# Optimization experiments

Hardware: AMD Instinct MI355X
Metric: run time of the kernel (lower is better)

Reference implementation:

```python
import jax, jax.numpy as jnp
import numpy as np

VOCAB, E, H, L, B, T, S, V = 32000, 512, 1024, 2, 64, 64, 128, 1024
LSTM_IN = 2 * E  # input_feed=True -> cat(embed, prev_output)


def setup_inputs() -> dict:
    key = jax.random.key(0)
    ks = jax.random.split(key, 12)
    s = lambda *d: 1.0 / np.sqrt(d[-1])
    return {
        "tgt_batch": jax.random.randint(ks[0], (T, B), 0, VOCAB),
        "h_encoder": jax.random.normal(ks[1], (B, S, V), jnp.float32),
        "emb": jax.random.normal(ks[2], (VOCAB, E), jnp.float32) * 0.02,
        "output_init": jnp.zeros((B, E), jnp.float32),
        "hidden_init": jnp.zeros((L, B, H), jnp.float32),
        "W_ih": jax.random.uniform(ks[3], (L, 4 * H, LSTM_IN), jnp.float32, -s(H), s(H)),
        "W_hh": jax.random.uniform(ks[4], (L, 4 * H, H), jnp.float32, -s(H), s(H)),
        "b_ih": jax.random.uniform(ks[5], (L, 4 * H), jnp.float32, -s(H), s(H)),
        "b_hh": jax.random.uniform(ks[6], (L, 4 * H), jnp.float32, -s(H), s(H)),
        "W1": jax.random.uniform(ks[7], (V, H), jnp.float32, -s(H), s(H)),   # query_size->values_size
        "b1": jnp.zeros((V,), jnp.float32),
        "W2": jax.random.uniform(ks[8], (E, H + V), jnp.float32, -s(H + V), s(H + V)),
        "b2": jnp.zeros((E,), jnp.float32),
    }


def reference(tgt_batch, h_encoder, emb, output_init, hidden_init,
              W_ih, W_hh, b_ih, b_hh, W1, b1, W2, b2):
    x_seq = emb[tgt_batch]  # [T, B, E]

    def lstm_cell(x, h, c):  # x:[B,2E], h/c:[L,B,H]
        hs, cs, inp = [], [], x
        for l in range(L):
            gates = inp @ W_ih[l].T + b_ih[l] + h[l] @ W_hh[l].T + b_hh[l]
            i, f, g, o = jnp.split(gates, 4, axis=-1)  # torch gate order i,f,g,o
            c_new = jax.nn.sigmoid(f) * c[l] + jax.nn.sigmoid(i) * jnp.tanh(g)
            h_new = jax.nn.sigmoid(o) * jnp.tanh(c_new)
            hs.append(h_new); cs.append(c_new); inp = h_new
        return jnp.stack(hs), jnp.stack(cs), inp

    def global_attn(query):  # query:[B,H]
        q = query @ W1.T + b1                              # [B,V]
        scores = jnp.einsum('bv,bsv->bs', q, h_encoder)    # [B,S]
        a = jax.nn.softmax(scores, axis=-1)
        attended = jnp.einsum('bs,bsv->bv', a, h_encoder)  # [B,V]
        return jnp.tanh(jnp.concatenate([attended, query], axis=-1) @ W2.T + b2)

    def step(carry, x):
        h, c, out = carry
        inp = jnp.concatenate([x, out], axis=-1)  # input feed
        h, c, top = lstm_cell(inp, h, c)
        o = global_attn(top)  # dropout is identity in eval mode
        return (h, c, o), o

    c0 = jnp.zeros_like(hidden_init)
    _, outs = jax.lax.scan(step, (hidden_init, c0, output_init), x_seq)
    return jnp.transpose(outs, (1, 0, 2))  # [B, T, E]
```

## Files before the change

kernel.cpp:

```cpp
#include <hip/hip_runtime.h>

typedef _Float16 f16;
typedef f16 f16x8 __attribute__((ext_vector_type(8)));
typedef f16 f16x2 __attribute__((ext_vector_type(2)));
typedef float f32x4 __attribute__((ext_vector_type(4)));
typedef unsigned long long u64;

#define MFMA16(a, b, c) __builtin_amdgcn_mfma_f32_16x16x32_f16(a, b, c, 0, 0, 0)
#define ROT 16

__device__ inline float fsig(float x) { return 1.f / (1.f + __expf(-x)); }
__device__ inline float ftanh(float x) {
    x = fminf(15.f, fmaxf(-15.f, x));
    float e = __expf(2.f * x);
    return (e - 1.f) / (e + 1.f);
}

__device__ __forceinline__ void bstore8(void* p, u64 v) {
    __hip_atomic_store((u64*)p, v, __ATOMIC_RELAXED, __HIP_MEMORY_SCOPE_AGENT);
}
__device__ __forceinline__ void bstore4(float* p, float v) {
    __hip_atomic_store(p, v, __ATOMIC_RELAXED, __HIP_MEMORY_SCOPE_AGENT);
}
__device__ __forceinline__ float bload_f32(const float* p) {
    return __hip_atomic_load((float*)p, __ATOMIC_RELAXED, __HIP_MEMORY_SCOPE_AGENT);
}
__device__ __forceinline__ void fstore_u32(unsigned* p, unsigned v) {
    __hip_atomic_store(p, v, __ATOMIC_RELAXED, __HIP_MEMORY_SCOPE_AGENT);
}
__device__ __forceinline__ unsigned fload_u32(unsigned* p) {
    return __hip_atomic_load(p, __ATOMIC_RELAXED, __HIP_MEMORY_SCOPE_AGENT);
}

__global__ __launch_bounds__(256) void k_convert(
    const float* __restrict__ Wih, const float* __restrict__ Whh,
    const float* __restrict__ W1, const float* __restrict__ W2,
    const float* __restrict__ bih, const float* __restrict__ bhh,
    const int* __restrict__ tgt, const float* __restrict__ emb,
    const float* __restrict__ henc,
    f16* __restrict__ wcat, f16* __restrict__ w1c, f16* __restrict__ w2a,
    f16* __restrict__ w2b, float* __restrict__ bsum, f16* __restrict__ Xall,
    f16* __restrict__ h16)
{
    const long NW = 16777216, NT = 1048576, NA = 524288, NB = 524288,
               NS = 8192, NX = 2097152, NH = 8388608;
    const long TOT = NW + NT + NA + NB + NS + NX + NH;
    for (long i = (long)blockIdx.x * 256 + threadIdx.x; i < TOT;
         i += (long)gridDim.x * 256) {
        if (i < NW) {
            long l = i >> 23;
            long r = i & 8388607;
            int j = (int)(r >> 11), k = (int)(r & 2047);
            float val = (k < 1024) ? Wih[(l * 4096 + j) * 1024 + k]
                                   : Whh[(l * 4096 + j) * 1024 + (k - 1024)];
            wcat[i] = (f16)val;
        } else if (i < NW + NT) {
            long r = i - NW;
            int h = (int)(r >> 10), v = (int)(r & 1023);
            w1c[r] = (f16)W1[(long)v * 1024 + h];
        } else if (i < NW + NT + NA) {
            long r = i - NW - NT;
            int e = (int)(r >> 10), v = (int)(r & 1023);
            w2a[r] = (f16)W2[(long)e * 2048 + v];
        } else if (i < NW + NT + NA + NB) {
            long r = i - NW - NT - NA;
            int e = (int)(r >> 10), k = (int)(r & 1023);
            w2b[r] = (f16)W2[(long)e * 2048 + 1024 + k];
        } else if (i < NW + NT + NA + NB + NS) {
            long r = i - NW - NT - NA - NB;
            bsum[r] = bih[r] + bhh[r];
        } else if (i < NW + NT + NA + NB + NS + NX) {
            long r = i - NW - NT - NA - NB - NS;
            int t = (int)(r >> 15), mm = (int)((r >> 9) & 63), k = (int)(r & 511);
            Xall[r] = (f16)emb[(long)tgt[t * 64 + mm] * 512 + k];
        } else {
            long r = i - NW - NT - NA - NB - NS - NX;
            h16[r] = (f16)henc[r];
        }
    }
}

__global__ __launch_bounds__(256) void k_init(
    const float* __restrict__ oinit, const float* __restrict__ hinit,
    f16* __restrict__ O0, f16* __restrict__ H00, f16* __restrict__ H10,
    float* __restrict__ c01, unsigned* __restrict__ sync)
{
    int idx = blockIdx.x * 256 + threadIdx.x;
    if (idx < 32768) {
        O0[idx] = (f16)oinit[idx];
    } else if (idx < 98304) {
        H00[idx - 32768] = (f16)hinit[idx - 32768];
    } else if (idx < 163840) {
        H10[idx - 98304] = (f16)hinit[65536 + (idx - 98304)];
    } else if (idx < 294912) {
        c01[idx - 163840] = 0.f;
    } else if (idx < 297984) {
        sync[idx - 294912] = 0u;
    }
}

__global__ __launch_bounds__(256) void k_sb(
    const float* __restrict__ b1, const float* __restrict__ henc,
    float* __restrict__ sb)
{
    int bs = blockIdx.x * 256 + threadIdx.x;
    const float* hr = henc + (long)bs * 1024;
    float a = 0.f;
    for (int k = 0; k < 1024; k += 4) {
        float4 h4 = *(const float4*)(hr + k);
        float4 b4 = *(const float4*)(b1 + k);
        a += h4.x * b4.x + h4.y * b4.y + h4.z * b4.z + h4.w * b4.w;
    }
    sb[bs] = a;
}

__global__ __launch_bounds__(256) void k_gemm(
    const f16* __restrict__ A, const f16* __restrict__ Bm,
    f16* __restrict__ C, int N)
{
    int nb = N >> 7;
    int bm = blockIdx.x / nb, bn = blockIdx.x % nb;
    int tid = threadIdx.x, w = tid >> 6, lane = tid & 63;
    int quad = lane >> 4, nn = lane & 15;
    const f16* ap = A + (long)(bm * 64 + w * 16 + nn) * 1024 + quad * 8;
    const f16* bp = Bm + (long)(bn * 128 + nn) * 1024 + quad * 8;
    f32x4 acc[8] = {};
    for (int kk = 0; kk < 1024; kk += 32) {
        f16x8 av = *(const f16x8*)(ap + kk);
        #pragma unroll
        for (int t2 = 0; t2 < 8; ++t2) {
            f16x8 bv = *(const f16x8*)(bp + (long)t2 * 16 * 1024 + kk);
            acc[t2] = MFMA16(av, bv, acc[t2]);
        }
    }
    #pragma unroll
    for (int t2 = 0; t2 < 8; ++t2)
        #pragma unroll
        for (int r = 0; r < 4; ++r) {
            int m = bm * 64 + w * 16 + quad * 4 + r;
            int col = bn * 128 + t2 * 16 + nn;
            C[(long)m * N + col] = (f16)acc[t2][r];
        }
}

__device__ __forceinline__ void gsync(unsigned* sync, unsigned e) {
    asm volatile("s_waitcnt vmcnt(0) lgkmcnt(0)" ::: "memory");
    __syncthreads();
    unsigned* arr = sync;
    unsigned* rel = sync + 256;
    if (threadIdx.x == 0)
        fstore_u32(arr + blockIdx.x, e);
    if (blockIdx.x == 0) {
        if (threadIdx.x < 64) {
            int lane = threadIdx.x;
            for (;;) {
                unsigned v0 = fload_u32(arr + lane);
                unsigned v1 = fload_u32(arr + 64 + lane);
                unsigned v2 = fload_u32(arr + 128 + lane);
                unsigned v3 = fload_u32(arr + 192 + lane);
                if (__all((int)(v0 >= e && v1 >= e && v2 >= e && v3 >= e)))
                    break;
                __builtin_amdgcn_s_sleep(1);
            }
            if (lane < 8) fstore_u32(rel + lane * 32, e);
        }
    } else if (threadIdx.x == 0) {
        unsigned* r = rel + (blockIdx.x & 7) * 32;
        while (fload_u32(r) < e)
            __builtin_amdgcn_s_sleep(2);
    }
    __syncthreads();
    asm volatile("" ::: "memory");
}

__device__ __forceinline__ void lstm_core(
    const f16* base, int rst, const f16x8* wreg,
    const float* __restrict__ bs_, float* __restrict__ c_,
    f16* __restrict__ dest, float* lds, int b, int tid)
{
    int w = tid >> 6, lane = tid & 63, quad = lane >> 4, n = lane & 15;
    const f16* ap = base + (long)n * rst + quad * 8;
    f32x4 acc0 = {}, acc1 = {}, acc2 = {}, acc3 = {};
    #pragma unroll
    for (int kk = 0; kk < 8; ++kk) {
        f16x8 bv = wreg[kk];
        f16x8 a0 = *(const f16x8*)(ap + kk * 32);
        f16x8 a1 = *(const f16x8*)(ap + (long)16 * rst + kk * 32);
        f16x8 a2 = *(const f16x8*)(ap + (long)32 * rst + kk * 32);
        f16x8 a3 = *(const f16x8*)(ap + (long)48 * rst + kk * 32);
        acc0 = MFMA16(a0, bv, acc0);
        acc1 = MFMA16(a1, bv, acc1);
        acc2 = MFMA16(a2, bv, acc2);
        acc3 = MFMA16(a3, bv, acc3);
    }
    #pragma unroll
    for (int r = 0; r < 4; ++r) {
        int mb = quad * 4 + r;
        lds[(w * 64 + mb) * 17 + n]      = acc0[r];
        lds[(w * 64 + 16 + mb) * 17 + n] = acc1[r];
        lds[(w * 64 + 32 + mb) * 17 + n] = acc2[r];
        lds[(w * 64 + 48 + mb) * 17 + n] = acc3[r];
    }
    __syncthreads();
    if (tid < 256) {
        int m = tid >> 2, uu = tid & 3;
        float s0 = 0.f, s1 = 0.f, s2 = 0.f, s3 = 0.f;
        #pragma unroll
        for (int ww = 0; ww < 8; ++ww) {
            const float* p = lds + (ww * 64 + m) * 17 + uu * 4;
            s0 += p[0]; s1 += p[1]; s2 += p[2]; s3 += p[3];
        }
        int ug = b * 4 + uu;
        float iv = fsig(s0 + bs_[ug]);
        float fv = fsig(s1 + bs_[1024 + ug]);
        float gv = ftanh(s2 + bs_[2048 + ug]);
        float ov = fsig(s3 + bs_[3072 + ug]);
        float cold = c_[m * 1024 + ug];
        float cn = fv * cold + iv * gv;
        float hn = ov * ftanh(cn);
        c_[m * 1024 + ug] = cn;
        lds[8704 + m * 4 + uu] = hn;
    }
    __syncthreads();
    if (tid < 64) {
        union { f16 h[4]; u64 u; } pk;
        #pragma unroll
        for (int uu = 0; uu < 4; ++uu) pk.h[uu] = (f16)lds[8704 + tid * 4 + uu];
        bstore8(dest + (long)tid * 1024 + b * 4, pk.u);
    }
}

__device__ __forceinline__ void z1q(
    const f16* __restrict__ H1n, f16x8 wz, const float* __restrict__ b2,
    float* __restrict__ Z1f, int er, int kq, float* lds, int tid)
{
    int w = tid >> 6, lane = tid & 63, quad = lane >> 4, n = lane & 15;
    const f16* ap = H1n + (long)n * 1024 + kq * 256 + w * 32 + quad * 8;
    f32x4 acc0 = {}, acc1 = {}, acc2 = {}, acc3 = {};
    f16x8 a0 = *(const f16x8*)(ap);
    f16x8 a1 = *(const f16x8*)(ap + 16384);
    f16x8 a2 = *(const f16x8*)(ap + 32768);
    f16x8 a3 = *(const f16x8*)(ap + 49152);
    acc0 = MFMA16(a0, wz, acc0);
    acc1 = MFMA16(a1, wz, acc1);
    acc2 = MFMA16(a2, wz, acc2);
    acc3 = MFMA16(a3, wz, acc3);
    #pragma unroll
    for (int r = 0; r < 4; ++r) {
        int mb = quad * 4 + r;
        lds[(w * 64 + mb) * 17 + n]      = acc0[r];
        lds[(w * 64 + 16 + mb) * 17 + n] = acc1[r];
        lds[(w * 64 + 32 + mb) * 17 + n] = acc2[r];
        lds[(w * 64 + 48 + mb) * 17 + n] = acc3[r];
    }
    __syncthreads();
    int mm = tid >> 3, n0 = (tid & 7) * 2;
    float s0 = 0.f, s1 = 0.f;
    #pragma unroll
    for (int ww = 0; ww < 8; ++ww) {
        const float* p = lds + (ww * 64 + mm) * 17 + n0;
        s0 += p[0]; s1 += p[1];
    }
    int e = er * 16 + n0;
    if (kq == 0) { s0 += b2[e]; s1 += b2[e + 1]; }
    union { float f[2]; u64 u; } pk;
    pk.f[0] = s0; pk.f[1] = s1;
    bstore8(Z1f + kq * 32768 + (long)mm * 512 + e, pk.u);
}

__global__ __launch_bounds__(512, 2) void k_persist(
    const f16* __restrict__ wcat, const float* __restrict__ bsum,
    float* __restrict__ c01, const f16* __restrict__ Xall,
    f16* __restrict__ Orot, f16* __restrict__ H0rot, f16* __restrict__ H1rot,
    const f16* __restrict__ P16, const f16* __restrict__ Q216,
    const f16* __restrict__ w2b, const float* __restrict__ sb,
    const float* __restrict__ b2, float* __restrict__ out,
    float* __restrict__ Z1f, float* __restrict__ Z2p,
    float* __restrict__ Z2s, unsigned* __restrict__ sync)
{
    extern __shared__ float smem[];
    float* scr = smem;
    f16* h1l = (f16*)(smem + 8960);
    f16* Pl  = (f16*)(smem + 9472);
    f16* Q2l = Pl + 32768;

    int b = blockIdx.x, tid = threadIdx.x;
    int m = b >> 2, sq = b & 3;
    int wv = tid >> 6, lane = tid & 63, quad = lane >> 4, nn = lane & 15;

    f16x8 w0[8], w1[8];
    {
        int j0 = (nn & 3) * 1024 + b * 4 + (nn >> 2);
        const f16* wp = wcat + (long)j0 * 2048 + wv * 256 + quad * 8;
        #pragma unroll
        for (int kk = 0; kk < 8; ++kk) {
            w0[kk] = *(const f16x8*)(wp + kk * 32);
            w1[kk] = *(const f16x8*)(wp + 8388608 + kk * 32);
        }
    }
    f16x8 wz = {};
    if (b < 128) {
        int er = b & 31, kq = b >> 5;
        const f16* zp = w2b + (long)(er * 16 + nn) * 1024 + kq * 256 + wv * 32 + quad * 8;
        wz = *(const f16x8*)zp;
    }
    {
        const uint4* gp = (const uint4*)(P16 + ((long)(m * 128 + sq * 32)) * 1024);
        #pragma unroll
        for (int i = 0; i < 8; ++i) ((uint4*)Pl)[i * 512 + tid] = gp[i * 512 + tid];
        const uint4* gq = (const uint4*)(Q216 + ((long)(m * 128 + sq * 32)) * 512);
        #pragma unroll
        for (int i = 0; i < 4; ++i) ((uint4*)Q2l)[i * 512 + tid] = gq[i * 512 + tid];
    }
    __syncthreads();

    unsigned epoch = 0;
    for (int t = 0; t < 64; ++t) {
        int rs0 = t & (ROT - 1), rs1 = (t + 1) & (ROT - 1);
        const f16* Xc = Xall + (long)t * 32768;
        const f16* Oc = Orot + (long)rs0 * 32768;
        const f16* H0c = H0rot + (long)rs0 * 65536;
        f16* H0n = H0rot + (long)rs1 * 65536;
        const f16* H1c = H1rot + (long)rs0 * 65536;
        f16* H1n = H1rot + (long)rs1 * 65536;

        {
            const f16* base; int rst;
            if (wv < 2)      { base = Xc + wv * 256;        rst = 512; }
            else if (wv < 4) { base = Oc + (wv - 2) * 256;  rst = 512; }
            else             { base = H0c + (wv - 4) * 256; rst = 1024; }
            lstm_core(base, rst, w0, bsum, c01, H0n, scr, b, tid);
        }
        gsync(sync, ++epoch);

        {
            const f16* base = (wv < 4) ? (H0n + wv * 256) : (H1c + (wv - 4) * 256);
            lstm_core(base, 1024, w1, bsum + 4096, c01 + 65536, H1n, scr, b, tid);
        }
        gsync(sync, ++epoch);

        {
            if (tid < 128)
                ((uint4*)h1l)[tid] = *(const uint4*)(H1n + (long)m * 1024 + tid * 8);
            if (b < 128)
                z1q(H1n, wz, b2, Z1f, b & 31, b >> 5, scr, tid);
            __syncthreads();
            int sl = tid >> 4, kc = tid & 15;
            const f16* prow = Pl + sl * 1024;
            float a0 = 0.f;
            #pragma unroll
            for (int i = 0; i < 8; ++i) {
                int ch = (i * 16 + kc) * 8;
                f16x8 pv = *(const f16x8*)(prow + ch);
                f16x8 hv = *(const f16x8*)(h1l + ch);
                #pragma unroll
                for (int p2 = 0; p2 < 4; ++p2) {
                    f16x2 pa = { pv[p2 * 2], pv[p2 * 2 + 1] };
                    f16x2 ha = { hv[p2 * 2], hv[p2 * 2 + 1] };
                    a0 = __builtin_amdgcn_fdot2(pa, ha, a0, false);
                }
            }
            #pragma unroll
            for (int off = 8; off; off >>= 1) a0 += __shfl_xor(a0, off, 16);
            if (kc == 0)
                scr[8704 + sl] = a0 + sb[m * 128 + sq * 32 + sl];
            __syncthreads();
            if (tid < 32) {
                float v = scr[8704 + tid];
                float mx = v;
                #pragma unroll
                for (int off = 16; off; off >>= 1) mx = fmaxf(mx, __shfl_xor(mx, off));
                float ev = __expf(v - mx);
                float sm = ev;
                #pragma unroll
                for (int off = 16; off; off >>= 1) sm += __shfl_xor(sm, off);
                scr[8704 + tid] = ev;
                if (tid == 0) {
                    union { float f[2]; u64 u; } pk;
                    pk.f[0] = mx; pk.f[1] = sm;
                    bstore8(Z2s + ((m * 4 + sq) << 1), pk.u);
                }
            }
            __syncthreads();
            float zp = 0.f;
            #pragma unroll 8
            for (int jy = 0; jy < 32; ++jy)
                zp += scr[8704 + jy] * (float)Q2l[jy * 512 + tid];
            bstore4(Z2p + ((m * 4 + sq) << 9) + tid, zp);
        }
        gsync(sync, ++epoch);

        {
            if (tid < 8) scr[8744 + tid] = bload_f32(Z2s + m * 8 + tid);
            __syncthreads();
            if (tid < 128) {
                float m0 = scr[8744], s0q = scr[8745], m1 = scr[8746], s1q = scr[8747],
                      m2 = scr[8748], s2q = scr[8749], m3 = scr[8750], s3q = scr[8751];
                float M = fmaxf(fmaxf(m0, m1), fmaxf(m2, m3));
                float q0 = __expf(m0 - M), q1 = __expf(m1 - M),
                      q2 = __expf(m2 - M), q3 = __expf(m3 - M);
                float den = q0 * s0q + q1 * s1q + q2 * s2q + q3 * s3q;
                int e = sq * 128 + tid;
                float z = bload_f32(Z1f + (m << 9) + e)
                        + bload_f32(Z1f + 32768 + (m << 9) + e)
                        + bload_f32(Z1f + 65536 + (m << 9) + e)
                        + bload_f32(Z1f + 98304 + (m << 9) + e);
                float num = q0 * bload_f32(Z2p + ((m * 4 + 0) << 9) + e)
                          + q1 * bload_f32(Z2p + ((m * 4 + 1) << 9) + e)
                          + q2 * bload_f32(Z2p + ((m * 4 + 2) << 9) + e)
                          + q3 * bload_f32(Z2p + ((m * 4 + 3) << 9) + e);
                z += num / den;
                float o = ftanh(z);
                out[((long)m * 64 + t) * 512 + e] = o;
                ((f16*)(scr + 8752))[tid] = (f16)o;
            }
            __syncthreads();
            if (tid < 32) {
                f16* ob = (f16*)(scr + 8752);
                union { f16 h[4]; u64 u; } pk;
                #pragma unroll
                for (int i = 0; i < 4; ++i) pk.h[i] = ob[tid * 4 + i];
                bstore8(Orot + (long)rs1 * 32768 + m * 512 + sq * 128 + tid * 4, pk.u);
            }
        }
        gsync(sync, ++epoch);
    }
}

extern "C" void kernel_launch(void* const* d_in, const int* in_sizes, int n_in,
                              void* d_out, int out_size, void* d_ws, size_t ws_size,
                              hipStream_t stream)
{
    const int*   tgt   = (const int*)d_in[0];
    const float* henc  = (const float*)d_in[1];
    const float* emb   = (const float*)d_in[2];
    const float* oinit = (const float*)d_in[3];
    const float* hinit = (const float*)d_in[4];
    const float* Wih   = (const float*)d_in[5];
    const float* Whh   = (const float*)d_in[6];
    const float* bih   = (const float*)d_in[7];
    const float* bhh   = (const float*)d_in[8];
    const float* W1    = (const float*)d_in[9];
    const float* b1    = (const float*)d_in[10];
    const float* W2    = (const float*)d_in[11];
    const float* b2    = (const float*)d_in[12];
    float* out = (float*)d_out;

    char* ws = (char*)d_ws;
    f16*      wcat  = (f16*)(ws + 0);
    f16*      P16   = (f16*)(ws + 33554432);
    f16*      Q216  = (f16*)(ws + 50331648);
    f16*      h16   = (f16*)(ws + 58720256);
    f16*      w2b   = (f16*)(ws + 75497472);
    f16*      w1c   = (f16*)(ws + 76546048);
    f16*      w2a   = (f16*)(ws + 78643200);
    f16*      Xall  = (f16*)(ws + 79691776);
    f16*      H0rot = (f16*)(ws + 83886080);
    f16*      H1rot = (f16*)(ws + 85983232);
    f16*      Orot  = (f16*)(ws + 88080384);
    float*    c01   = (float*)(ws + 89128960);
    float*    Z1f   = (float*)(ws + 58720256);
    float*    Z2p   = (float*)(ws + 59244544);
    float*    Z2s   = (float*)(ws + 90439680);
    float*    bsum  = (float*)(ws + 90472448);
    float*    sb    = (float*)(ws + 90505216);
    unsigned* sync  = (unsigned*)(ws + 90537984);

    hipLaunchKernelGGL(k_convert, dim3(4096), dim3(256), 0, stream,
                       Wih, Whh, W1, W2, bih, bhh, tgt, emb, henc,
                       wcat, w1c, w2a, w2b, bsum, Xall, h16);
    hipLaunchKernelGGL(k_init, dim3(1164), dim3(256), 0, stream,
                       oinit, hinit, Orot, H0rot, H1rot, c01, sync);
    hipLaunchKernelGGL(k_sb, dim3(32), dim3(256), 0, stream, b1, henc, sb);
    hipLaunchKernelGGL(k_gemm, dim3(128 * 8), dim3(256), 0, stream,
                       h16, w1c, P16, 1024);
    hipLaunchKernelGGL(k_gemm, dim3(128 * 4), dim3(256), 0, stream,
                       h16, w2a, Q216, 512);

    static const unsigned LDS_BYTES = 9472 * 4 + 32768 * 2 + 16384 * 2;
    hipFuncSetAttribute((const void*)k_persist,
                        hipFuncAttributeMaxDynamicSharedMemorySize, LDS_BYTES);
    void* args[] = { &wcat, &bsum, &c01, &Xall, &Orot, &H0rot, &H1rot, &P16,
                     &Q216, &w2b, &sb, &b2, &out, &Z1f, &Z2p, &Z2s, &sync };
    hipLaunchCooperativeKernel((const void*)k_persist, dim3(256), dim3(512),
                               args, LDS_BYTES, stream);
}
```

Baseline: 2.234 ms.

## Replace third grid barrier with per-batch group flags and local W2 dot

The grid-wide sync after the attention partials is replaced by a flag barrier among only the four blocks that share a batch row. The Z1 projection (W2 times h1) is now computed per block with fdot2 from the LDS copy of h1 and global W2 rows, instead of through MFMA in 128 blocks with a global Z1f exchange. This cuts one full grid barrier per timestep. In exchange, each block reads a W2 slice from global memory every step and does more scalar dot work.

```diff
diff --git a/kernel.cpp b/kernel.cpp
--- a/kernel.cpp
+++ b/kernel.cpp
@@ -30,6 +30,15 @@
 }
 __device__ __forceinline__ unsigned fload_u32(unsigned* p) {
     return __hip_atomic_load(p, __ATOMIC_RELAXED, __HIP_MEMORY_SCOPE_AGENT);
+}
+
+__device__ __forceinline__ void poll4(unsigned* f, unsigned e, int lane) {
+    for (;;) {
+        unsigned v = fload_u32(f + (lane & 3));
+        if (__all((int)(v >= e))) break;
+        __builtin_amdgcn_s_sleep(1);
+    }
+    asm volatile("" ::: "memory");
 }
 
 __global__ __launch_bounds__(256) void k_convert(
@@ -230,44 +239,6 @@
     }
 }
 
-__device__ __forceinline__ void z1q(
-    const f16* __restrict__ H1n, f16x8 wz, const float* __restrict__ b2,
-    float* __restrict__ Z1f, int er, int kq, float* lds, int tid)
-{
-    int w = tid >> 6, lane = tid & 63, quad = lane >> 4, n = lane & 15;
-    const f16* ap = H1n + (long)n * 1024 + kq * 256 + w * 32 + quad * 8;
-    f32x4 acc0 = {}, acc1 = {}, acc2 = {}, acc3 = {};
-    f16x8 a0 = *(const f16x8*)(ap);
-    f16x8 a1 = *(const f16x8*)(ap + 16384);
-    f16x8 a2 = *(const f16x8*)(ap + 32768);
-    f16x8 a3 = *(const f16x8*)(ap + 49152);
-    acc0 = MFMA16(a0, wz, acc0);
-    acc1 = MFMA16(a1, wz, acc1);
-    acc2 = MFMA16(a2, wz, acc2);
-    acc3 = MFMA16(a3, wz, acc3);
-    #pragma unroll
-    for (int r = 0; r < 4; ++r) {
-        int mb = quad * 4 + r;
-        lds[(w * 64 + mb) * 17 + n]      = acc0[r];
-        lds[(w * 64 + 16 + mb) * 17 + n] = acc1[r];
-        lds[(w * 64 + 32 + mb) * 17 + n] = acc2[r];
-        lds[(w * 64 + 48 + mb) * 17 + n] = acc3[r];
-    }
-    __syncthreads();
-    int mm = tid >> 3, n0 = (tid & 7) * 2;
-    float s0 = 0.f, s1 = 0.f;
-    #pragma unroll
-    for (int ww = 0; ww < 8; ++ww) {
-        const float* p = lds + (ww * 64 + mm) * 17 + n0;
-        s0 += p[0]; s1 += p[1];
-    }
-    int e = er * 16 + n0;
-    if (kq == 0) { s0 += b2[e]; s1 += b2[e + 1]; }
-    union { float f[2]; u64 u; } pk;
-    pk.f[0] = s0; pk.f[1] = s1;
-    bstore8(Z1f + kq * 32768 + (long)mm * 512 + e, pk.u);
-}
-
 __global__ __launch_bounds__(512, 2) void k_persist(
     const f16* __restrict__ wcat, const float* __restrict__ bsum,
     float* __restrict__ c01, const f16* __restrict__ Xall,
@@ -275,8 +246,8 @@
     const f16* __restrict__ P16, const f16* __restrict__ Q216,
     const f16* __restrict__ w2b, const float* __restrict__ sb,
     const float* __restrict__ b2, float* __restrict__ out,
-    float* __restrict__ Z1f, float* __restrict__ Z2p,
-    float* __restrict__ Z2s, unsigned* __restrict__ sync)
+    float* __restrict__ Z2p, float* __restrict__ Z2s,
+    unsigned* __restrict__ sync)
 {
     extern __shared__ float smem[];
     float* scr = smem;
@@ -287,6 +258,7 @@
     int b = blockIdx.x, tid = threadIdx.x;
     int m = b >> 2, sq = b & 3;
     int wv = tid >> 6, lane = tid & 63, quad = lane >> 4, nn = lane & 15;
+    unsigned* ggf = sync + 1024;
 
     f16x8 w0[8], w1[8];
     {
@@ -297,12 +269,6 @@
             w0[kk] = *(const f16x8*)(wp + kk * 32);
             w1[kk] = *(const f16x8*)(wp + 8388608 + kk * 32);
         }
-    }
-    f16x8 wz = {};
-    if (b < 128) {
-        int er = b & 31, kq = b >> 5;
-        const f16* zp = w2b + (long)(er * 16 + nn) * 1024 + kq * 256 + wv * 32 + quad * 8;
-        wz = *(const f16x8*)zp;
     }
     {
         const uint4* gp = (const uint4*)(P16 + ((long)(m * 128 + sq * 32)) * 1024);
@@ -342,9 +308,30 @@
         {
             if (tid < 128)
                 ((uint4*)h1l)[tid] = *(const uint4*)(H1n + (long)m * 1024 + tid * 8);
-            if (b < 128)
-                z1q(H1n, wz, b2, Z1f, b & 31, b >> 5, scr, tid);
-            __syncthreads();
+            __syncthreads();
+
+            {
+                int el = tid >> 2, kq = tid & 3;
+                int eg = sq * 128 + el;
+                const f16* wp2 = w2b + (long)eg * 1024 + kq * 256;
+                const f16* hp = h1l + kq * 256;
+                float z1 = 0.f;
+                #pragma unroll 8
+                for (int i = 0; i < 32; ++i) {
+                    f16x8 wv8 = *(const f16x8*)(wp2 + i * 8);
+                    f16x8 hv8 = *(const f16x8*)(hp + i * 8);
+                    #pragma unroll
+                    for (int p2 = 0; p2 < 4; ++p2) {
+                        f16x2 wa = { wv8[p2 * 2], wv8[p2 * 2 + 1] };
+                        f16x2 ha = { hv8[p2 * 2], hv8[p2 * 2 + 1] };
+                        z1 = __builtin_amdgcn_fdot2(wa, ha, z1, false);
+                    }
+                }
+                z1 += __shfl_xor(z1, 1);
+                z1 += __shfl_xor(z1, 2);
+                if (kq == 0) scr[8736 + el] = z1 + b2[eg];
+            }
+
             int sl = tid >> 4, kc = tid & 15;
             const f16* prow = Pl + sl * 1024;
             float a0 = 0.f;
@@ -365,6 +352,7 @@
             if (kc == 0)
                 scr[8704 + sl] = a0 + sb[m * 128 + sq * 32 + sl];
             __syncthreads();
+
             if (tid < 32) {
                 float v = scr[8704 + tid];
                 float mx = v;
@@ -382,41 +370,41 @@
                 }
             }
             __syncthreads();
+
             float zp = 0.f;
             #pragma unroll 8
             for (int jy = 0; jy < 32; ++jy)
                 zp += scr[8704 + jy] * (float)Q2l[jy * 512 + tid];
             bstore4(Z2p + ((m * 4 + sq) << 9) + tid, zp);
-        }
-        gsync(sync, ++epoch);
-
-        {
-            if (tid < 8) scr[8744 + tid] = bload_f32(Z2s + m * 8 + tid);
+
+            asm volatile("s_waitcnt vmcnt(0)" ::: "memory");
+            __syncthreads();
+            if (tid == 0) fstore_u32(ggf + m * 32 + sq, (unsigned)(t + 1));
+            if (tid < 64) poll4(ggf + m * 32, (unsigned)(t + 1), tid);
+            __syncthreads();
+
+            if (tid < 8) scr[8864 + tid] = bload_f32(Z2s + m * 8 + tid);
             __syncthreads();
             if (tid < 128) {
-                float m0 = scr[8744], s0q = scr[8745], m1 = scr[8746], s1q = scr[8747],
-                      m2 = scr[8748], s2q = scr[8749], m3 = scr[8750], s3q = scr[8751];
+                float m0 = scr[8864], s0q = scr[8865], m1 = scr[8866], s1q = scr[8867],
+                      m2 = scr[8868], s2q = scr[8869], m3 = scr[8870], s3q = scr[8871];
                 float M = fmaxf(fmaxf(m0, m1), fmaxf(m2, m3));
                 float q0 = __expf(m0 - M), q1 = __expf(m1 - M),
                       q2 = __expf(m2 - M), q3 = __expf(m3 - M);
                 float den = q0 * s0q + q1 * s1q + q2 * s2q + q3 * s3q;
-                int e = sq * 128 + tid;
-                float z = bload_f32(Z1f + (m << 9) + e)
-                        + bload_f32(Z1f + 32768 + (m << 9) + e)
-                        + bload_f32(Z1f + 65536 + (m << 9) + e)
-                        + bload_f32(Z1f + 98304 + (m << 9) + e);
-                float num = q0 * bload_f32(Z2p + ((m * 4 + 0) << 9) + e)
-                          + q1 * bload_f32(Z2p + ((m * 4 + 1) << 9) + e)
-                          + q2 * bload_f32(Z2p + ((m * 4 + 2) << 9) + e)
-                          + q3 * bload_f32(Z2p + ((m * 4 + 3) << 9) + e);
-                z += num / den;
+                int e2 = sq * 128 + tid;
+                float num = q0 * bload_f32(Z2p + ((m * 4 + 0) << 9) + e2)
+                          + q1 * bload_f32(Z2p + ((m * 4 + 1) << 9) + e2)
+                          + q2 * bload_f32(Z2p + ((m * 4 + 2) << 9) + e2)
+                          + q3 * bload_f32(Z2p + ((m * 4 + 3) << 9) + e2);
+                float z = scr[8736 + tid] + num / den;
                 float o = ftanh(z);
-                out[((long)m * 64 + t) * 512 + e] = o;
-                ((f16*)(scr + 8752))[tid] = (f16)o;
+                out[((long)m * 64 + t) * 512 + e2] = o;
+                ((f16*)(scr + 8880))[tid] = (f16)o;
             }
             __syncthreads();
             if (tid < 32) {
-                f16* ob = (f16*)(scr + 8752);
+                f16* ob = (f16*)(scr + 8880);
                 union { f16 h[4]; u64 u; } pk;
                 #pragma unroll
                 for (int i = 0; i < 4; ++i) pk.h[i] = ob[tid * 4 + i];
@@ -459,8 +447,7 @@
     f16*      H1rot = (f16*)(ws + 85983232);
     f16*      Orot  = (f16*)(ws + 88080384);
     float*    c01   = (float*)(ws + 89128960);
-    float*    Z1f   = (float*)(ws + 58720256);
-    float*    Z2p   = (float*)(ws + 59244544);
+    float*    Z2p   = (float*)(ws + 58720256);
     float*    Z2s   = (float*)(ws + 90439680);
     float*    bsum  = (float*)(ws + 90472448);
     float*    sb    = (float*)(ws + 90505216);
@@ -481,7 +468,7 @@
     hipFuncSetAttribute((const void*)k_persist,
                         hipFuncAttributeMaxDynamicSharedMemorySize, LDS_BYTES);
     void* args[] = { &wcat, &bsum, &c01, &Xall, &Orot, &H0rot, &H1rot, &P16,
-                     &Q216, &w2b, &sb, &b2, &out, &Z1f, &Z2p, &Z2s, &sync };
+                     &Q216, &w2b, &sb, &b2, &out, &Z2p, &Z2s, &sync };
     hipLaunchCooperativeKernel((const void*)k_persist, dim3(256), dim3(512),
                                args, LDS_BYTES, stream);
 }
```

New measurement: 2.549 ms. 1.14x slower.
